# Kernel optimization log

Measured on AMD Instinct MI355X. Metric: run time of the kernel, lower is better.

Reference implementation:

```python
import jax, jax.numpy as jnp
import numpy as np

D_MODEL = 1024
N_HEADS = 16
D_HEAD = D_MODEL // N_HEADS


def setup_inputs() -> dict:
    key = jax.random.key(0)
    ks = jax.random.split(key, 5)
    s_in = 1.0 / np.sqrt(D_MODEL)
    x = jax.random.normal(ks[0], (2, 2048, D_MODEL), dtype=jnp.float32)
    W_qkv = jax.random.uniform(ks[1], (D_MODEL, 3 * D_MODEL), jnp.float32, -s_in, s_in)
    b_qkv = jax.random.uniform(ks[2], (3 * D_MODEL,), jnp.float32, -s_in, s_in)
    W_out = jax.random.uniform(ks[3], (D_MODEL, D_MODEL), jnp.float32, -s_in, s_in)
    b_out = jax.random.uniform(ks[4], (D_MODEL,), jnp.float32, -s_in, s_in)
    return {"x": x, "W_qkv": W_qkv, "b_qkv": b_qkv, "W_out": W_out, "b_out": b_out}


def reference(x, W_qkv, b_qkv, W_out, b_out):
    B, T, C = x.shape
    qkv = x @ W_qkv + b_qkv                      # [B,T,3C]
    q, k, v = jnp.split(qkv, 3, axis=-1)
    # [B,T,C] -> [B,H,T,Dh]
    def heads(t):
        return t.reshape(B, T, N_HEADS, D_HEAD).transpose(0, 2, 1, 3)
    q, k, v = heads(q), heads(k), heads(v)
    att = jnp.einsum('bhqd,bhkd->bhqk', q, k) / np.sqrt(D_HEAD).astype(np.float32)
    causal = jnp.tril(jnp.ones((T, T), dtype=bool))  # True = keep
    att = jnp.where(causal, att, -jnp.inf)
    att = jax.nn.softmax(att, axis=-1)
    y = jnp.einsum('bhqk,bhkd->bhqd', att, v)    # [B,H,T,Dh]
    y = y.transpose(0, 2, 1, 3).reshape(B, T, C)
    y = y @ W_out + b_out
    return (y, att)
```

## Files before the change

### kernel.cpp

```cpp
#include <hip/hip_runtime.h>

#define B_ 2
#define T_ 2048
#define C_ 1024
#define H_ 16
#define DH_ 64
#define N3_ 3072
#define BT_ 4096

typedef __attribute__((ext_vector_type(4))) float f32x4;
typedef __attribute__((ext_vector_type(8))) short short8;
typedef __attribute__((ext_vector_type(4))) unsigned short us4;

__device__ __forceinline__ unsigned short f2bf(float f) {
  return __builtin_bit_cast(unsigned short, (__bf16)f);
}

__device__ __forceinline__ float bf2f(unsigned short s) {
  unsigned int u = ((unsigned int)s) << 16;
  return __builtin_bit_cast(float, u);
}

__device__ __forceinline__ void gload16(const void* g, void* l) {
  __builtin_amdgcn_global_load_lds(
      (const __attribute__((address_space(1))) unsigned int*)g,
      (__attribute__((address_space(3))) unsigned int*)l, 16, 0, 0);
}

__device__ __forceinline__ void lds_barrier() {
  asm volatile("s_waitcnt lgkmcnt(0)" ::: "memory");
  __builtin_amdgcn_s_barrier();
}

#define QSCALE 0.1803368801111137f

__global__ __launch_bounds__(256) void prep_kernel(const float* __restrict__ x,
                                                   const float* __restrict__ W_qkv,
                                                   const float* __restrict__ W_out,
                                                   unsigned short* __restrict__ xb,
                                                   unsigned short* __restrict__ wqkvT,
                                                   unsigned short* __restrict__ woutT) {
  __shared__ float tile[32][33];
  int b = blockIdx.x;
  if (b < 4096) {
    size_t i = (size_t)b * 256 + threadIdx.x;
    float4 v = *(const float4*)(x + i * 4);
    us4 o = {f2bf(v.x), f2bf(v.y), f2bf(v.z), f2bf(v.w)};
    *(us4*)(xb + i * 4) = o;
    return;
  }
  const float* W;
  unsigned short* Wt;
  int Ncols, bx, by;
  if (b < 4096 + 3072) {
    int bb = b - 4096;
    W = W_qkv; Wt = wqkvT; Ncols = 3072; bx = bb % 96; by = bb / 96;
  } else {
    int bb = b - 7168;
    W = W_out; Wt = woutT; Ncols = 1024; bx = bb % 32; by = bb / 32;
  }
  int n0 = bx * 32, k0 = by * 32;
  int tx = threadIdx.x & 31, ty = threadIdx.x >> 5;
#pragma unroll
  for (int i = 0; i < 4; ++i) {
    int k = k0 + ty + i * 8;
    tile[ty + i * 8][tx] = W[(size_t)k * Ncols + n0 + tx];
  }
  __syncthreads();
#pragma unroll
  for (int i = 0; i < 4; ++i) {
    int n = n0 + ty + i * 8;
    Wt[(size_t)n * 1024 + k0 + tx] = f2bf(tile[tx][ty + i * 8]);
  }
}

template <int MODE, int BN>
__global__ __launch_bounds__(256) void gemm_kernel(
    const unsigned short* __restrict__ A, const unsigned short* __restrict__ Bt,
    const float* __restrict__ bias, unsigned short* __restrict__ q_ws,
    unsigned short* __restrict__ k_ws, unsigned short* __restrict__ vt_ws,
    float* __restrict__ yout) {
  __shared__ unsigned short lds_a[128 * 32];
  __shared__ unsigned short lds_b[BN * 32];
  const int tid = threadIdx.x;
  const int w = tid >> 6, l = tid & 63;
  const int m0 = blockIdx.y * 128;
  const int n0 = blockIdx.x * BN;
  const int wr = (w >> 1) * 64, wc = (w & 1) * (BN / 2);
  constexpr int NI = BN / 32;
  const int K = 1024;

  f32x4 acc[4][NI] = {};
  for (int k0 = 0; k0 < K; k0 += 32) {
    __syncthreads();
#pragma unroll
    for (int i = 0; i < 2; ++i) {
      int li = i * 256 + tid;
      int row = li >> 2, cl = li & 3, cs = cl ^ (row & 3);
      gload16((const char*)A + ((size_t)(m0 + row) * K + k0) * 2 + cs * 16,
              (char*)lds_a + li * 16);
    }
#pragma unroll
    for (int i = 0; i < BN / 64; ++i) {
      int li = i * 256 + tid;
      int row = li >> 2, cl = li & 3, cs = cl ^ (row & 3);
      gload16((const char*)Bt + ((size_t)(n0 + row) * K + k0) * 2 + cs * 16,
              (char*)lds_b + li * 16);
    }
    __syncthreads();
    short8 af[4], bfr[NI];
#pragma unroll
    for (int mi = 0; mi < 4; ++mi) {
      int m = wr + mi * 16 + (l & 15);
      af[mi] = *(const short8*)((const char*)lds_a + m * 64 + (((l >> 4) ^ (m & 3)) * 16));
    }
#pragma unroll
    for (int ni = 0; ni < NI; ++ni) {
      int n = wc + ni * 16 + (l & 15);
      bfr[ni] = *(const short8*)((const char*)lds_b + n * 64 + (((l >> 4) ^ (n & 3)) * 16));
    }
#pragma unroll
    for (int mi = 0; mi < 4; ++mi)
#pragma unroll
      for (int ni = 0; ni < NI; ++ni)
        acc[mi][ni] = __builtin_amdgcn_mfma_f32_16x16x32_bf16(af[mi], bfr[ni], acc[mi][ni], 0, 0, 0);
  }

  float bi[NI];
#pragma unroll
  for (int ni = 0; ni < NI; ++ni) bi[ni] = bias[n0 + wc + ni * 16 + (l & 15)];

  if (MODE == 1) {
#pragma unroll
    for (int mi = 0; mi < 4; ++mi) {
#pragma unroll
      for (int ni = 0; ni < NI; ++ni) {
        int n = n0 + wc + ni * 16 + (l & 15);
#pragma unroll
        for (int r = 0; r < 4; ++r) {
          int m = m0 + wr + mi * 16 + ((l >> 4) << 2) + r;
          yout[(size_t)m * 1024 + n] = acc[mi][ni][r] + bi[ni];
        }
      }
    }
  } else {
    int sec = (n0 + wc) >> 10;
#pragma unroll
    for (int mi = 0; mi < 4; ++mi) {
#pragma unroll
      for (int ni = 0; ni < NI; ++ni) {
        int n = n0 + wc + ni * 16 + (l & 15);
        int nn = n & 1023, h = nn >> 6, d = nn & 63;
        if (sec == 2) {
          int mbase = m0 + wr + mi * 16 + ((l >> 4) << 2);
          int bb = mbase >> 11, t = mbase & 2047;
          us4 o;
#pragma unroll
          for (int r = 0; r < 4; ++r) o[r] = f2bf(acc[mi][ni][r] + bi[ni]);
          *(us4*)(vt_ws + ((size_t)(bb * 16 + h) * 64 + d) * 2048 + t) = o;
        } else {
#pragma unroll
          for (int r = 0; r < 4; ++r) {
            int m = m0 + wr + mi * 16 + ((l >> 4) << 2) + r;
            int bb = m >> 11, t = m & 2047;
            float v = acc[mi][ni][r] + bi[ni];
            size_t idx = ((size_t)(bb * 16 + h) * 2048 + t) * 64 + d;
            if (sec == 0)
              q_ws[idx] = f2bf(v * QSCALE);
            else
              k_ws[idx] = f2bf(v);
          }
        }
      }
    }
  }
}

__global__ __launch_bounds__(512) void attn_kernel(
    const unsigned short* __restrict__ q_ws, const unsigned short* __restrict__ k_ws,
    const unsigned short* __restrict__ vt_ws, float* __restrict__ att,
    unsigned short* __restrict__ yh) {
  __shared__ unsigned short lds_k[64 * 64];
  __shared__ unsigned short lds_v[64 * 64];
  __shared__ unsigned short lds_p[128 * 72];
  const int tid = threadIdx.x, w = tid >> 6, l = tid & 63;
  const int id = blockIdx.x;
  const int rr = id >> 8, j = id & 255;
  int qt = j & 15;
  if (rr) qt = 15 - qt;
  const int bh = (j >> 4) + (rr << 4);
  const int q0 = qt * 128;
  const size_t hoff = (size_t)bh * (2048 * 64);
  const char* kbase = (const char*)k_ws + hoff * 2;
  const char* vbase = (const char*)vt_ws + hoff * 2;

  auto stageK = [&](int kt) {
    int row = tid >> 3, cl = tid & 7, cs = cl ^ (row & 7);
    gload16(kbase + (size_t)kt * 8192 + row * 128 + cs * 16, (char*)lds_k + tid * 16);
  };
  auto stageV = [&](int kt) {
    int row = tid >> 3, cl = tid & 7, cs = cl ^ (row & 7);
    gload16(vbase + (size_t)row * 4096 + kt * 128 + cs * 16, (char*)lds_v + tid * 16);
  };

  short8 qf[2];
  {
    int row = q0 + w * 16 + (l & 15);
    const char* qb = (const char*)q_ws + (hoff + (size_t)row * 64) * 2;
    qf[0] = *(const short8*)(qb + ((l >> 4) * 16));
    qf[1] = *(const short8*)(qb + 64 + ((l >> 4) * 16));
  }

  const int rowbase = q0 + w * 16 + ((l >> 4) << 2);
  const int nkt = 2 * qt + 2;

  float lsum[4] = {0.f, 0.f, 0.f, 0.f};
  auto step1 = [&](int kt, bool diag) {
    lds_barrier();
    stageK(kt);
    __syncthreads();
    f32x4 s[4] = {};
#pragma unroll
    for (int ni = 0; ni < 4; ++ni) {
      int jj = ni * 16 + (l & 15);
#pragma unroll
      for (int cc = 0; cc < 2; ++cc) {
        short8 bf = *(const short8*)((const char*)lds_k + jj * 128 +
                                     (((cc * 4 + (l >> 4)) ^ (jj & 7)) * 16));
        s[ni] = __builtin_amdgcn_mfma_f32_16x16x32_bf16(qf[cc], bf, s[ni], 0, 0, 0);
      }
    }
#pragma unroll
    for (int ni = 0; ni < 4; ++ni) {
#pragma unroll
      for (int r = 0; r < 4; ++r) {
        float e = __builtin_exp2f(s[ni][r]);
        if (diag) {
          int colg = kt * 64 + ni * 16 + (l & 15);
          if (colg > rowbase + r) e = 0.f;
        }
        lsum[r] += e;
      }
    }
  };
  for (int kt = 0; kt < 2 * qt; ++kt) step1(kt, false);
  step1(2 * qt, true);
  step1(2 * qt + 1, true);

  float invl[4];
#pragma unroll
  for (int r = 0; r < 4; ++r) {
    float t = lsum[r];
    t += __shfl_xor(t, 1);
    t += __shfl_xor(t, 2);
    t += __shfl_xor(t, 4);
    t += __shfl_xor(t, 8);
    invl[r] = 1.0f / t;
  }

  f32x4 yacc[4] = {};
  float* attb = att + (size_t)bh * 2048 * 2048;
  auto step2 = [&](int kt, bool diag) {
    lds_barrier();
    stageK(kt);
    stageV(kt);
    __syncthreads();
    f32x4 s[4] = {};
#pragma unroll
    for (int ni = 0; ni < 4; ++ni) {
      int jj = ni * 16 + (l & 15);
#pragma unroll
      for (int cc = 0; cc < 2; ++cc) {
        short8 bf = *(const short8*)((const char*)lds_k + jj * 128 +
                                     (((cc * 4 + (l >> 4)) ^ (jj & 7)) * 16));
        s[ni] = __builtin_amdgcn_mfma_f32_16x16x32_bf16(qf[cc], bf, s[ni], 0, 0, 0);
      }
    }
#pragma unroll
    for (int ni = 0; ni < 4; ++ni) {
#pragma unroll
      for (int r = 0; r < 4; ++r) {
        float p = __builtin_exp2f(s[ni][r]) * invl[r];
        if (diag) {
          int colg = kt * 64 + ni * 16 + (l & 15);
          if (colg > rowbase + r) p = 0.f;
        }
        lds_p[(w * 16 + ((l >> 4) << 2) + r) * 72 + ni * 16 + (l & 15)] = f2bf(p);
      }
    }
    lds_barrier();
#pragma unroll
    for (int cc = 0; cc < 2; ++cc) {
      int prow = w * 16 + (l & 15);
      short8 pf = *(const short8*)((const char*)lds_p + prow * 144 + cc * 64 + ((l >> 4) * 16));
      float* ad = attb + (size_t)(q0 + prow) * 2048 + kt * 64 + cc * 32 + ((l >> 4) * 8);
      float4 v0 = make_float4(bf2f((unsigned short)pf[0]), bf2f((unsigned short)pf[1]),
                              bf2f((unsigned short)pf[2]), bf2f((unsigned short)pf[3]));
      float4 v1 = make_float4(bf2f((unsigned short)pf[4]), bf2f((unsigned short)pf[5]),
                              bf2f((unsigned short)pf[6]), bf2f((unsigned short)pf[7]));
      *(float4*)ad = v0;
      *(float4*)(ad + 4) = v1;
#pragma unroll
      for (int ni = 0; ni < 4; ++ni) {
        int d = ni * 16 + (l & 15);
        short8 vf = *(const short8*)((const char*)lds_v + d * 128 +
                                     (((cc * 4 + (l >> 4)) ^ (d & 7)) * 16));
        yacc[ni] = __builtin_amdgcn_mfma_f32_16x16x32_bf16(pf, vf, yacc[ni], 0, 0, 0);
      }
    }
  };
  for (int kt = 0; kt < 2 * qt; ++kt) step2(kt, false);
  step2(2 * qt, true);
  step2(2 * qt + 1, true);

  {
    int bb = bh >> 4, h = bh & 15;
#pragma unroll
    for (int ni = 0; ni < 4; ++ni) {
      int d = ni * 16 + (l & 15);
#pragma unroll
      for (int r = 0; r < 4; ++r) {
        int t = rowbase + r;
        yh[((size_t)bb * 2048 + t) * 1024 + h * 64 + d] = f2bf(yacc[ni][r]);
      }
    }
  }

  int cstart = q0 + 128;
  if (cstart < 2048) {
    int nz = 2048 - cstart;
    float4 z = make_float4(0.f, 0.f, 0.f, 0.f);
    for (int row = 0; row < 128; ++row) {
      float* dst = attb + (size_t)(q0 + row) * 2048 + cstart;
      for (int c = tid * 4; c < nz; c += 2048) *(float4*)(dst + c) = z;
    }
  }
}

extern "C" void kernel_launch(void* const* d_in, const int* in_sizes, int n_in,
                              void* d_out, int out_size, void* d_ws, size_t ws_size,
                              hipStream_t stream) {
  const float* x = (const float*)d_in[0];
  const float* W_qkv = (const float*)d_in[1];
  const float* b_qkv = (const float*)d_in[2];
  const float* W_out = (const float*)d_in[3];
  const float* b_out = (const float*)d_in[4];
  float* out = (float*)d_out;

  char* ws = (char*)d_ws;
  unsigned short* xb = (unsigned short*)(ws);
  unsigned short* wqkvT = (unsigned short*)(ws + 8388608);
  unsigned short* woutT = (unsigned short*)(ws + 14680064);
  unsigned short* q_ws = (unsigned short*)(ws + 16777216);
  unsigned short* k_ws = (unsigned short*)(ws + 25165824);
  unsigned short* vt_ws = (unsigned short*)(ws + 33554432);
  unsigned short* yh_ws = (unsigned short*)(ws + 41943040);

  float* y_out = out;
  float* att_out = out + (size_t)BT_ * C_;

  prep_kernel<<<8192, 256, 0, stream>>>(x, W_qkv, W_out, xb, wqkvT, woutT);
  gemm_kernel<0, 128><<<dim3(24, 32), 256, 0, stream>>>(xb, wqkvT, b_qkv, q_ws, k_ws, vt_ws,
                                                        nullptr);
  attn_kernel<<<512, 512, 0, stream>>>(q_ws, k_ws, vt_ws, att_out, yh_ws);
  gemm_kernel<1, 64><<<dim3(16, 32), 256, 0, stream>>>(yh_ws, woutT, b_out, nullptr, nullptr,
                                                       nullptr, y_out);
}
```

Before: 249.8 us.

## Double-buffer K/V tiles in attention with prefetch and MFMA priority

Converts both attention passes (row-sum pass and probability/PV pass) to double-buffered LDS tiles for K and V. The next tile is prefetched with global_load_lds while the current one is computed, so global load latency overlaps the matrix work instead of stalling at each barrier. A vmcnt-based barrier waits only for the prefetch loads, not the attention-matrix stores issued after them. It also raises wave priority around the MFMA sections. The cost is twice the K/V LDS footprint, which may reduce occupancy.

```diff
diff --git a/kernel.cpp b/kernel.cpp
--- a/kernel.cpp
+++ b/kernel.cpp
@@ -31,6 +31,12 @@
   asm volatile("s_waitcnt lgkmcnt(0)" ::: "memory");
   __builtin_amdgcn_s_barrier();
 }
+
+#define VM_BARRIER(N)                                        \
+  do {                                                       \
+    asm volatile("s_waitcnt vmcnt(" #N ")" ::: "memory");    \
+    __builtin_amdgcn_s_barrier();                            \
+  } while (0)
 
 #define QSCALE 0.1803368801111137f
 
@@ -180,8 +186,8 @@
     const unsigned short* __restrict__ q_ws, const unsigned short* __restrict__ k_ws,
     const unsigned short* __restrict__ vt_ws, float* __restrict__ att,
     unsigned short* __restrict__ yh) {
-  __shared__ unsigned short lds_k[64 * 64];
-  __shared__ unsigned short lds_v[64 * 64];
+  __shared__ unsigned short lds_k[2][64 * 64];
+  __shared__ unsigned short lds_v[2][64 * 64];
   __shared__ unsigned short lds_p[128 * 72];
   const int tid = threadIdx.x, w = tid >> 6, l = tid & 63;
   const int id = blockIdx.x;
@@ -194,13 +200,13 @@
   const char* kbase = (const char*)k_ws + hoff * 2;
   const char* vbase = (const char*)vt_ws + hoff * 2;
 
-  auto stageK = [&](int kt) {
+  auto stageK = [&](int kt, int buf) {
     int row = tid >> 3, cl = tid & 7, cs = cl ^ (row & 7);
-    gload16(kbase + (size_t)kt * 8192 + row * 128 + cs * 16, (char*)lds_k + tid * 16);
+    gload16(kbase + (size_t)kt * 8192 + row * 128 + cs * 16, (char*)lds_k[buf] + tid * 16);
   };
-  auto stageV = [&](int kt) {
+  auto stageV = [&](int kt, int buf) {
     int row = tid >> 3, cl = tid & 7, cs = cl ^ (row & 7);
-    gload16(vbase + (size_t)row * 4096 + kt * 128 + cs * 16, (char*)lds_v + tid * 16);
+    gload16(vbase + (size_t)row * 4096 + kt * 128 + cs * 16, (char*)lds_v[buf] + tid * 16);
   };
 
   short8 qf[2];
@@ -215,21 +221,25 @@
   const int nkt = 2 * qt + 2;
 
   float lsum[4] = {0.f, 0.f, 0.f, 0.f};
-  auto step1 = [&](int kt, bool diag) {
-    lds_barrier();
-    stageK(kt);
-    __syncthreads();
+  stageK(0, 0);
+  VM_BARRIER(0);
+  for (int kt = 0; kt < nkt; ++kt) {
+    const int cur = kt & 1;
+    if (kt + 1 < nkt) stageK(kt + 1, cur ^ 1);
+    const bool diag = (kt >= 2 * qt);
     f32x4 s[4] = {};
+    __builtin_amdgcn_s_setprio(1);
 #pragma unroll
     for (int ni = 0; ni < 4; ++ni) {
       int jj = ni * 16 + (l & 15);
 #pragma unroll
       for (int cc = 0; cc < 2; ++cc) {
-        short8 bf = *(const short8*)((const char*)lds_k + jj * 128 +
+        short8 bf = *(const short8*)((const char*)lds_k[cur] + jj * 128 +
                                      (((cc * 4 + (l >> 4)) ^ (jj & 7)) * 16));
         s[ni] = __builtin_amdgcn_mfma_f32_16x16x32_bf16(qf[cc], bf, s[ni], 0, 0, 0);
       }
     }
+    __builtin_amdgcn_s_setprio(0);
 #pragma unroll
     for (int ni = 0; ni < 4; ++ni) {
 #pragma unroll
@@ -242,10 +252,8 @@
         lsum[r] += e;
       }
     }
-  };
-  for (int kt = 0; kt < 2 * qt; ++kt) step1(kt, false);
-  step1(2 * qt, true);
-  step1(2 * qt + 1, true);
+    if (kt + 1 < nkt) VM_BARRIER(0);
+  }
 
   float invl[4];
 #pragma unroll
@@ -260,22 +268,26 @@
 
   f32x4 yacc[4] = {};
   float* attb = att + (size_t)bh * 2048 * 2048;
-  auto step2 = [&](int kt, bool diag) {
-    lds_barrier();
-    stageK(kt);
-    stageV(kt);
-    __syncthreads();
+  stageK(0, 0);
+  stageV(0, 0);
+  VM_BARRIER(0);
+  for (int kt = 0; kt < nkt; ++kt) {
+    const int cur = kt & 1;
+    if (kt + 1 < nkt) { stageK(kt + 1, cur ^ 1); stageV(kt + 1, cur ^ 1); }
+    const bool diag = (kt >= 2 * qt);
     f32x4 s[4] = {};
+    __builtin_amdgcn_s_setprio(1);
 #pragma unroll
     for (int ni = 0; ni < 4; ++ni) {
       int jj = ni * 16 + (l & 15);
 #pragma unroll
       for (int cc = 0; cc < 2; ++cc) {
-        short8 bf = *(const short8*)((const char*)lds_k + jj * 128 +
+        short8 bf = *(const short8*)((const char*)lds_k[cur] + jj * 128 +
                                      (((cc * 4 + (l >> 4)) ^ (jj & 7)) * 16));
         s[ni] = __builtin_amdgcn_mfma_f32_16x16x32_bf16(qf[cc], bf, s[ni], 0, 0, 0);
       }
     }
+    __builtin_amdgcn_s_setprio(0);
 #pragma unroll
     for (int ni = 0; ni < 4; ++ni) {
 #pragma unroll
@@ -300,18 +312,18 @@
                               bf2f((unsigned short)pf[6]), bf2f((unsigned short)pf[7]));
       *(float4*)ad = v0;
       *(float4*)(ad + 4) = v1;
+      __builtin_amdgcn_s_setprio(1);
 #pragma unroll
       for (int ni = 0; ni < 4; ++ni) {
         int d = ni * 16 + (l & 15);
-        short8 vf = *(const short8*)((const char*)lds_v + d * 128 +
+        short8 vf = *(const short8*)((const char*)lds_v[cur] + d * 128 +
                                      (((cc * 4 + (l >> 4)) ^ (d & 7)) * 16));
         yacc[ni] = __builtin_amdgcn_mfma_f32_16x16x32_bf16(pf, vf, yacc[ni], 0, 0, 0);
       }
-    }
-  };
-  for (int kt = 0; kt < 2 * qt; ++kt) step2(kt, false);
-  step2(2 * qt, true);
-  step2(2 * qt + 1, true);
+      __builtin_amdgcn_s_setprio(0);
+    }
+    if (kt + 1 < nkt) VM_BARRIER(4);
+  }
 
   {
     int bb = bh >> 4, h = bh & 15;
```

Result: no change. 252.5 us (+1.1%).

## Compute transposed scores and repack P via lane shuffles instead of LDS

Applied to the files above, without the earlier changes.

Swaps the MFMA operand order so each lane holds four consecutive key columns of one query row. This lets each lane write its probabilities to the attention output as a full-precision float4 directly, instead of round-tripping through bf16 in LDS. The P operand for the PV MFMA is now built with packed bf16 conversions and cross-lane shuffles, which removes the LDS P buffer and one barrier per tile. The row-sum reduction also simplifies to two shuffles. The trade-off is extra shuffle and select instructions per tile and a changed global store pattern for the attention matrix.

```diff
diff --git a/kernel.cpp b/kernel.cpp
--- a/kernel.cpp
+++ b/kernel.cpp
@@ -11,6 +11,7 @@
 typedef __attribute__((ext_vector_type(4))) float f32x4;
 typedef __attribute__((ext_vector_type(8))) short short8;
 typedef __attribute__((ext_vector_type(4))) unsigned short us4;
+typedef __attribute__((ext_vector_type(4))) unsigned int u32x4;
 
 __device__ __forceinline__ unsigned short f2bf(float f) {
   return __builtin_bit_cast(unsigned short, (__bf16)f);
@@ -19,6 +20,12 @@
 __device__ __forceinline__ float bf2f(unsigned short s) {
   unsigned int u = ((unsigned int)s) << 16;
   return __builtin_bit_cast(float, u);
+}
+
+__device__ __forceinline__ unsigned int cvtpk(float a, float b) {
+  unsigned int r;
+  asm("v_cvt_pk_bf16_f32 %0, %1, %2" : "=v"(r) : "v"(a), "v"(b));
+  return r;
 }
 
 __device__ __forceinline__ void gload16(const void* g, void* l) {
@@ -182,7 +189,6 @@
     unsigned short* __restrict__ yh) {
   __shared__ unsigned short lds_k[64 * 64];
   __shared__ unsigned short lds_v[64 * 64];
-  __shared__ unsigned short lds_p[128 * 72];
   const int tid = threadIdx.x, w = tid >> 6, l = tid & 63;
   const int id = blockIdx.x;
   const int rr = id >> 8, j = id & 255;
@@ -211,10 +217,10 @@
     qf[1] = *(const short8*)(qb + 64 + ((l >> 4) * 16));
   }
 
-  const int rowbase = q0 + w * 16 + ((l >> 4) << 2);
-  const int nkt = 2 * qt + 2;
-
-  float lsum[4] = {0.f, 0.f, 0.f, 0.f};
+  const int qrow = q0 + w * 16 + (l & 15);
+  const int kcolbase = (l >> 4) << 2;
+
+  float lsum = 0.f;
   auto step1 = [&](int kt, bool diag) {
     lds_barrier();
     stageK(kt);
@@ -225,9 +231,9 @@
       int jj = ni * 16 + (l & 15);
 #pragma unroll
       for (int cc = 0; cc < 2; ++cc) {
-        short8 bf = *(const short8*)((const char*)lds_k + jj * 128 +
+        short8 kf = *(const short8*)((const char*)lds_k + jj * 128 +
                                      (((cc * 4 + (l >> 4)) ^ (jj & 7)) * 16));
-        s[ni] = __builtin_amdgcn_mfma_f32_16x16x32_bf16(qf[cc], bf, s[ni], 0, 0, 0);
+        s[ni] = __builtin_amdgcn_mfma_f32_16x16x32_bf16(kf, qf[cc], s[ni], 0, 0, 0);
       }
     }
 #pragma unroll
@@ -236,10 +242,10 @@
       for (int r = 0; r < 4; ++r) {
         float e = __builtin_exp2f(s[ni][r]);
         if (diag) {
-          int colg = kt * 64 + ni * 16 + (l & 15);
-          if (colg > rowbase + r) e = 0.f;
+          int colg = kt * 64 + ni * 16 + kcolbase + r;
+          if (colg > qrow) e = 0.f;
         }
-        lsum[r] += e;
+        lsum += e;
       }
     }
   };
@@ -247,19 +253,16 @@
   step1(2 * qt, true);
   step1(2 * qt + 1, true);
 
-  float invl[4];
-#pragma unroll
-  for (int r = 0; r < 4; ++r) {
-    float t = lsum[r];
-    t += __shfl_xor(t, 1);
-    t += __shfl_xor(t, 2);
-    t += __shfl_xor(t, 4);
-    t += __shfl_xor(t, 8);
-    invl[r] = 1.0f / t;
-  }
+  lsum += __shfl_xor(lsum, 16);
+  lsum += __shfl_xor(lsum, 32);
+  const float invl = 1.0f / lsum;
 
   f32x4 yacc[4] = {};
   float* attb = att + (size_t)bh * 2048 * 2048;
+  const int srcA = (l & 15) + ((l >> 4) & 1) * 32;
+  const int srcB = srcA + 16;
+  const bool hiSel = ((l >> 4) >> 1) & 1;
+
   auto step2 = [&](int kt, bool diag) {
     lds_barrier();
     stageK(kt);
@@ -271,40 +274,41 @@
       int jj = ni * 16 + (l & 15);
 #pragma unroll
       for (int cc = 0; cc < 2; ++cc) {
-        short8 bf = *(const short8*)((const char*)lds_k + jj * 128 +
+        short8 kf = *(const short8*)((const char*)lds_k + jj * 128 +
                                      (((cc * 4 + (l >> 4)) ^ (jj & 7)) * 16));
-        s[ni] = __builtin_amdgcn_mfma_f32_16x16x32_bf16(qf[cc], bf, s[ni], 0, 0, 0);
-      }
-    }
-#pragma unroll
-    for (int ni = 0; ni < 4; ++ni) {
+        s[ni] = __builtin_amdgcn_mfma_f32_16x16x32_bf16(kf, qf[cc], s[ni], 0, 0, 0);
+      }
+    }
+    unsigned int W0[4], W1[4];
+#pragma unroll
+    for (int ni = 0; ni < 4; ++ni) {
+      f32x4 p;
 #pragma unroll
       for (int r = 0; r < 4; ++r) {
-        float p = __builtin_exp2f(s[ni][r]) * invl[r];
+        float v = __builtin_exp2f(s[ni][r]) * invl;
         if (diag) {
-          int colg = kt * 64 + ni * 16 + (l & 15);
-          if (colg > rowbase + r) p = 0.f;
+          int colg = kt * 64 + ni * 16 + kcolbase + r;
+          if (colg > qrow) v = 0.f;
         }
-        lds_p[(w * 16 + ((l >> 4) << 2) + r) * 72 + ni * 16 + (l & 15)] = f2bf(p);
-      }
-    }
-    lds_barrier();
-#pragma unroll
-    for (int cc = 0; cc < 2; ++cc) {
-      int prow = w * 16 + (l & 15);
-      short8 pf = *(const short8*)((const char*)lds_p + prow * 144 + cc * 64 + ((l >> 4) * 16));
-      float* ad = attb + (size_t)(q0 + prow) * 2048 + kt * 64 + cc * 32 + ((l >> 4) * 8);
-      float4 v0 = make_float4(bf2f((unsigned short)pf[0]), bf2f((unsigned short)pf[1]),
-                              bf2f((unsigned short)pf[2]), bf2f((unsigned short)pf[3]));
-      float4 v1 = make_float4(bf2f((unsigned short)pf[4]), bf2f((unsigned short)pf[5]),
-                              bf2f((unsigned short)pf[6]), bf2f((unsigned short)pf[7]));
-      *(float4*)ad = v0;
-      *(float4*)(ad + 4) = v1;
+        p[r] = v;
+      }
+      *(f32x4*)(attb + (size_t)qrow * 2048 + kt * 64 + ni * 16 + kcolbase) = p;
+      W0[ni] = cvtpk(p[0], p[1]);
+      W1[ni] = cvtpk(p[2], p[3]);
+    }
+#pragma unroll
+    for (int kk = 0; kk < 2; ++kk) {
+      unsigned int a0 = __shfl(W0[2 * kk], srcA), a0b = __shfl(W0[2 * kk + 1], srcA);
+      unsigned int a1 = __shfl(W1[2 * kk], srcA), a1b = __shfl(W1[2 * kk + 1], srcA);
+      unsigned int b0 = __shfl(W0[2 * kk], srcB), b0b = __shfl(W0[2 * kk + 1], srcB);
+      unsigned int b1 = __shfl(W1[2 * kk], srcB), b1b = __shfl(W1[2 * kk + 1], srcB);
+      u32x4 F = {hiSel ? a0b : a0, hiSel ? a1b : a1, hiSel ? b0b : b0, hiSel ? b1b : b1};
+      short8 pf = __builtin_bit_cast(short8, F);
 #pragma unroll
       for (int ni = 0; ni < 4; ++ni) {
         int d = ni * 16 + (l & 15);
         short8 vf = *(const short8*)((const char*)lds_v + d * 128 +
-                                     (((cc * 4 + (l >> 4)) ^ (d & 7)) * 16));
+                                     (((kk * 4 + (l >> 4)) ^ (d & 7)) * 16));
         yacc[ni] = __builtin_amdgcn_mfma_f32_16x16x32_bf16(pf, vf, yacc[ni], 0, 0, 0);
       }
     }
@@ -320,7 +324,7 @@
       int d = ni * 16 + (l & 15);
 #pragma unroll
       for (int r = 0; r < 4; ++r) {
-        int t = rowbase + r;
+        int t = q0 + w * 16 + ((l >> 4) << 2) + r;
         yh[((size_t)bb * 2048 + t) * 1024 + h * 64 + d] = f2bf(yacc[ni][r]);
       }
     }
```

New measurement: 242.7 us. -2.8%, faster.
